# Performance work log

Hardware: AMD Instinct MI355X
Metric: run time of the kernel (lower is better)

The kernel has to match this reference:

```python
import jax, jax.numpy as jnp
import numpy as np

# Arbitrary non-contiguous kernel tap offsets (constructor arg sk_ind)
SK_IND = np.array([-512, -256, -128, -96, -64, -48, -32, -24, -16, -12, -8, -6,
                   -4, -3, -2, -1, 0, 1, 2, 3, 4, 6, 8, 12, 16, 24, 32, 48,
                   64, 96, 128, 256], dtype=np.int32)
IN_CHANNELS = 64
OUT_CHANNELS = 64
BATCH = 16
INPUT_LEN = 4096


def setup_inputs() -> dict:
    key = jax.random.key(0)
    k1, k2 = jax.random.split(key)
    x = jax.random.normal(k1, (BATCH, IN_CHANNELS, INPUT_LEN), dtype=jnp.float32)
    sk_weights = jax.random.normal(k2, (OUT_CHANNELS, IN_CHANNELS, SK_IND.shape[0]), dtype=jnp.float32)
    return {"x": x, "sk_weights": sk_weights}


def reference(x, sk_weights):
    # x: [B, Cin, L]; sk_weights: [Cout, Cin, K]
    B, C, L = x.shape
    low_pad = max(-int(SK_IND.min()), 0)   # zeros consumed by negative taps
    high_pad = max(int(SK_IND.max()), 0)   # zeros consumed by positive taps
    # Original pads zeros AFTER the signal: [x, zeros(high_pad), zeros(low_pad)];
    # negative numpy indices then wrap into the trailing low_pad zeros.
    padded = jnp.concatenate([x, jnp.zeros((B, C, high_pad + low_pad), x.dtype)], axis=-1)
    padded_len = L + high_pad + low_pad
    idx = SK_IND[:, None] + np.arange(L)                 # [K, L], static
    idx = np.where(idx < 0, padded_len + idx, idx)       # emulate numpy negative-index wrap
    gathered = padded[:, :, idx]                          # [B, Cin, K, L]
    # Per-position GEMM: contract over (Cin, K)
    return jnp.einsum('oik,bikl->bol', sk_weights, gathered)  # [B, Cout, L]
```

## Files before the change

kernel.cpp:

```cpp
#include <hip/hip_runtime.h>


#define B_    16
#define CIN   64
#define COUT  64
#define LEN   4096
#define PAD_LO 512
#define PAD_HI 256
#define LPAD  (LEN + PAD_LO + PAD_HI)
#define NTAP  32

typedef float f32x4 __attribute__((ext_vector_type(4)));
typedef short bf16x8_s __attribute__((ext_vector_type(8)));
typedef __bf16 bf16x8_b __attribute__((ext_vector_type(8)));
typedef unsigned short u16x8 __attribute__((ext_vector_type(8)));

template <typename V>
static __device__ inline auto mfma_16x16x32_bf16(V a, V b, f32x4 c, int)
    -> decltype(__builtin_amdgcn_mfma_f32_16x16x32_bf16(a, b, c, 0, 0, 0)) {
  return __builtin_amdgcn_mfma_f32_16x16x32_bf16(a, b, c, 0, 0, 0);
}
template <typename V>
static __device__ inline f32x4 mfma_16x16x32_bf16(V a, V b, f32x4 c, long) {
  return __builtin_amdgcn_mfma_f32_16x16x32_bf16(
      __builtin_bit_cast(bf16x8_b, a), __builtin_bit_cast(bf16x8_b, b), c, 0, 0, 0);
}

static __device__ inline unsigned short f32_to_bf16_rne(float f) {
  unsigned int u = __builtin_bit_cast(unsigned int, f);
  u += 0x7fffu + ((u >> 16) & 1u);
  return (unsigned short)(u >> 16);
}

static __device__ inline void async_copy16(const void* g, void* l) {
  __builtin_amdgcn_global_load_lds((const __attribute__((address_space(1))) unsigned int*)g,
                                   (__attribute__((address_space(3))) unsigned int*)l, 16, 0, 0);
}

__global__ __launch_bounds__(256) void prep_x(const float* __restrict__ x,
                                              unsigned short* __restrict__ xp) {
  __shared__ float tile[64][65];
  const int b = blockIdx.y;
  const int lp0 = blockIdx.x * 64;
  const int tid = threadIdx.x;
  const bool data = (lp0 >= PAD_LO) && (lp0 < PAD_LO + LEN);
  if (data) {
    const int l0 = lp0 - PAD_LO;
#pragma unroll
    for (int it = 0; it < 4; ++it) {
      const int pidx = it * 256 + tid;
      const int il = pidx >> 4;
      const int lq = (pidx & 15) * 4;
      const float4 v = *(const float4*)&x[(size_t)(b * CIN + il) * LEN + l0 + lq];
      tile[lq + 0][il] = v.x;
      tile[lq + 1][il] = v.y;
      tile[lq + 2][il] = v.z;
      tile[lq + 3][il] = v.w;
    }
  }
  __syncthreads();
#pragma unroll
  for (int it = 0; it < 2; ++it) {
    const int pidx = it * 256 + tid;
    const int ll = pidx >> 3;
    const int i8 = (pidx & 7) * 8;
    u16x8 v = {0, 0, 0, 0, 0, 0, 0, 0};
    if (data) {
#pragma unroll
      for (int j = 0; j < 8; ++j) v[j] = f32_to_bf16_rne(tile[ll][i8 + j]);
    }
    *(u16x8*)&xp[(size_t)(b * LPAD + lp0 + ll) * CIN + i8] = v;
  }
}

__global__ __launch_bounds__(256) void prep_w(const float* __restrict__ w,
                                              unsigned short* __restrict__ wf) {
  const int e = blockIdx.x * 256 + threadIdx.x;
  const int j = e & 7;
  const int lane = (e >> 3) & 63;
  const int m = (e >> 9) & 3;
  const int c = (e >> 11) & 1;
  const int t = e >> 12;
  const int q = lane >> 4, r = lane & 15;
  const int o = m * 16 + r;
  const int i = c * 32 + q * 8 + j;
  wf[e] = f32_to_bf16_rne(w[(size_t)(o * CIN + i) * NTAP + t]);
}

__global__ __launch_bounds__(256, 2) void sconv_main(const unsigned short* __restrict__ xp,
                                                     const unsigned short* __restrict__ wf,
                                                     float* __restrict__ out) {
  constexpr int TAP[NTAP] = {-512, -256, -128, -96, -64, -48, -32, -24, -16, -12, -8,
                             -6,   -4,   -3,   -2,  -1,  0,   1,   2,   3,   4,  6,
                             8,    12,   16,   24,  32,  48,  64,  96,  128, 256};
  __shared__ alignas(16) char smem[81920];

  const int id = blockIdx.x;
  const int b = (id & 7) * 2 + ((id >> 3) & 1);
  const int l0 = (id >> 4) * 128;
  const int lb = l0 + PAD_LO;
  const int tid = threadIdx.x;
  const int wv = tid >> 6, lane = tid & 63;
  const int q = lane >> 4, r = lane & 15;
  const int lh = wv & 1, ch = wv >> 1;

  const char* xbase = (const char*)xp + ((size_t)b * LPAD + lb) * (CIN * 2);
  const char* wbase = (const char*)wf;

  auto stageW = [&](int t) {
    const char* src = wbase + t * 8192;
    char* dst = smem + 65536 + (t & 1) * 8192;
#pragma unroll
    for (int it = 0; it < 2; ++it)
      async_copy16(src + (it * 256 + wv * 64 + lane) * 16,
                   dst + (it * 256 + wv * 64) * 16);
  };
  auto stageB = [&](int a0, int ng) {
    for (int g = wv; g < ng; g += 4) {
      const int ra = a0 + g * 8 + (lane >> 3);
      const int cs = (lane & 7) ^ (ra & 7);
      const int sb = (lb + a0 + g * 8) & 511;
      async_copy16(xbase + (ptrdiff_t)ra * 128 + cs * 16, smem + sb * 128);
    }
  };

  f32x4 acc[4][4] = {};

  stageW(0);
  stageB(-512, 16);

#pragma unroll
  for (int t = 0; t < NTAP; ++t) {
    __syncthreads();
    if (t + 1 < NTAP) {
      stageW(t + 1);
      const int dstart = TAP[t] + 128;
      const int dend = TAP[t + 1] + 128;
      const int a0 = dstart & ~7;
      stageB(a0, (dend - a0 + 7) >> 3);
    }
    __builtin_amdgcn_sched_barrier(0);

    const int e = (TAP[t] + r) & 7;
    const char* Wb = smem + 65536 + (t & 1) * 8192 + ch * 4096;
    bf16x8_s A[4], Bf[4];
#pragma unroll
    for (int m = 0; m < 4; ++m)
      A[m] = *(const bf16x8_s*)(Wb + m * 1024 + lane * 16);
#pragma unroll
    for (int n = 0; n < 4; ++n) {
      const int slot = (lb + TAP[t] + lh * 64 + 16 * n + r) & 511;
      Bf[n] = *(const bf16x8_s*)(smem + slot * 128 + (((ch * 4 + q) ^ e) << 4));
    }
#pragma unroll
    for (int m = 0; m < 4; ++m)
#pragma unroll
      for (int n = 0; n < 4; ++n)
        acc[m][n] = mfma_16x16x32_bf16(A[m], Bf[n], acc[m][n], 0);
  }

  __syncthreads();
  if (ch == 1) {
#pragma unroll
    for (int m = 0; m < 4; ++m)
#pragma unroll
      for (int n = 0; n < 4; ++n)
        *(f32x4*)(smem + lh * 16384 + ((m * 4 + n) * 64 + lane) * 16) = acc[m][n];
  }
  __syncthreads();
  if (ch == 0) {
#pragma unroll
    for (int m = 0; m < 4; ++m)
#pragma unroll
      for (int n = 0; n < 4; ++n) {
        const f32x4 other = *(const f32x4*)(smem + lh * 16384 + ((m * 4 + n) * 64 + lane) * 16);
        const f32x4 v = acc[m][n] + other;
#pragma unroll
        for (int d = 0; d < 4; ++d) {
          const int o = 16 * m + 4 * q + d;
          const int l = l0 + lh * 64 + 16 * n + r;
          out[((size_t)b * COUT + o) * LEN + l] = v[d];
        }
      }
  }
}

extern "C" void kernel_launch(void* const* d_in, const int* in_sizes, int n_in,
                              void* d_out, int out_size, void* d_ws, size_t ws_size,
                              hipStream_t stream) {
  const float* x = (const float*)d_in[0];
  const float* w = (const float*)d_in[1];
  float* out = (float*)d_out;

  unsigned short* xp = (unsigned short*)d_ws;
  unsigned short* wfp = xp + (size_t)B_ * LPAD * CIN;

  prep_x<<<dim3(LPAD / 64, B_), 256, 0, stream>>>(x, xp);
  prep_w<<<dim3((NTAP * 2 * 4 * 64 * 8) / 256), 256, 0, stream>>>(w, wfp);
  sconv_main<<<dim3(16 * 32), 256, 0, stream>>>(xp, wfp, out);
}
```

Before: 92.50 us.

## Use larger 256-position tiles with register double-buffered fragments and deeper prefetch

Each block now covers 256 output positions with 8 waves instead of 128 positions with 4 waves, using a 1024-row LDS ring for the shifted input rows. The weight and halo prefetch runs two taps ahead, and the LDS fragment reads for the next tap are loaded into a second register set while the current tap's MFMAs issue. The goal is to hide LDS read latency behind the matrix ops and to reduce redundant halo loads per output. The cost is about 144KB of LDS per block, which allows only one block per CU, plus higher register pressure from the doubled fragment sets.

```diff
diff --git a/kernel.cpp b/kernel.cpp
--- a/kernel.cpp
+++ b/kernel.cpp
@@ -9,6 +9,7 @@
 #define PAD_HI 256
 #define LPAD  (LEN + PAD_LO + PAD_HI)
 #define NTAP  32
+#define WOFF  131072
 
 typedef float f32x4 __attribute__((ext_vector_type(4)));
 typedef short bf16x8_s __attribute__((ext_vector_type(8)));
@@ -87,76 +88,80 @@
   wf[e] = f32_to_bf16_rne(w[(size_t)(o * CIN + i) * NTAP + t]);
 }
 
-__global__ __launch_bounds__(256, 2) void sconv_main(const unsigned short* __restrict__ xp,
+__global__ __launch_bounds__(512, 2) void sconv_main(const unsigned short* __restrict__ xp,
                                                      const unsigned short* __restrict__ wf,
                                                      float* __restrict__ out) {
   constexpr int TAP[NTAP] = {-512, -256, -128, -96, -64, -48, -32, -24, -16, -12, -8,
                              -6,   -4,   -3,   -2,  -1,  0,   1,   2,   3,   4,  6,
                              8,    12,   16,   24,  32,  48,  64,  96,  128, 256};
-  __shared__ alignas(16) char smem[81920];
+  __shared__ alignas(16) char smem[WOFF + 16384];
 
   const int id = blockIdx.x;
-  const int b = (id & 7) * 2 + ((id >> 3) & 1);
-  const int l0 = (id >> 4) * 128;
+  const int b = (id & 7) * 2 + (id >> 7);
+  const int l0 = ((id >> 3) & 15) * 256;
   const int lb = l0 + PAD_LO;
   const int tid = threadIdx.x;
   const int wv = tid >> 6, lane = tid & 63;
   const int q = lane >> 4, r = lane & 15;
-  const int lh = wv & 1, ch = wv >> 1;
+  const int lh = wv >> 1, ch = wv & 1;
 
   const char* xbase = (const char*)xp + ((size_t)b * LPAD + lb) * (CIN * 2);
   const char* wbase = (const char*)wf;
 
   auto stageW = [&](int t) {
-    const char* src = wbase + t * 8192;
-    char* dst = smem + 65536 + (t & 1) * 8192;
-#pragma unroll
-    for (int it = 0; it < 2; ++it)
-      async_copy16(src + (it * 256 + wv * 64 + lane) * 16,
-                   dst + (it * 256 + wv * 64) * 16);
+    async_copy16(wbase + t * 8192 + (wv * 64 + lane) * 16,
+                 smem + WOFF + (t & 1) * 8192 + wv * 1024);
   };
   auto stageB = [&](int a0, int ng) {
-    for (int g = wv; g < ng; g += 4) {
+    for (int g = wv; g < ng; g += 8) {
       const int ra = a0 + g * 8 + (lane >> 3);
       const int cs = (lane & 7) ^ (ra & 7);
-      const int sb = (lb + a0 + g * 8) & 511;
+      const int sb = (lb + a0 + g * 8) & 1023;
       async_copy16(xbase + (ptrdiff_t)ra * 128 + cs * 16, smem + sb * 128);
     }
   };
 
   f32x4 acc[4][4] = {};
+  bf16x8_s Ab[2][4], Bb[2][4];
+
+  auto readFrags = [&](int tt, int p) {
+    const char* Wb = smem + WOFF + (tt & 1) * 8192 + ch * 4096;
+#pragma unroll
+    for (int m = 0; m < 4; ++m)
+      Ab[p][m] = *(const bf16x8_s*)(Wb + m * 1024 + lane * 16);
+    const int e = (TAP[tt] + r) & 7;
+#pragma unroll
+    for (int n = 0; n < 4; ++n) {
+      const int slot = (lb + TAP[tt] + lh * 64 + 16 * n + r) & 1023;
+      Bb[p][n] = *(const bf16x8_s*)(smem + slot * 128 + (((ch * 4 + q) ^ e) << 4));
+    }
+  };
 
   stageW(0);
-  stageB(-512, 16);
+  stageW(1);
+  stageB(-512, 64);
+  __syncthreads();
+  readFrags(0, 0);
 
 #pragma unroll
   for (int t = 0; t < NTAP; ++t) {
     __syncthreads();
-    if (t + 1 < NTAP) {
-      stageW(t + 1);
-      const int dstart = TAP[t] + 128;
-      const int dend = TAP[t + 1] + 128;
+    if (t + 2 < NTAP) {
+      stageW(t + 2);
+      const int dstart = TAP[t + 1] + 256;
+      const int dend = TAP[t + 2] + 256;
       const int a0 = dstart & ~7;
       stageB(a0, (dend - a0 + 7) >> 3);
     }
     __builtin_amdgcn_sched_barrier(0);
-
-    const int e = (TAP[t] + r) & 7;
-    const char* Wb = smem + 65536 + (t & 1) * 8192 + ch * 4096;
-    bf16x8_s A[4], Bf[4];
-#pragma unroll
-    for (int m = 0; m < 4; ++m)
-      A[m] = *(const bf16x8_s*)(Wb + m * 1024 + lane * 16);
-#pragma unroll
-    for (int n = 0; n < 4; ++n) {
-      const int slot = (lb + TAP[t] + lh * 64 + 16 * n + r) & 511;
-      Bf[n] = *(const bf16x8_s*)(smem + slot * 128 + (((ch * 4 + q) ^ e) << 4));
-    }
+    if (t + 1 < NTAP) readFrags(t + 1, (t + 1) & 1);
+    __builtin_amdgcn_sched_barrier(0);
+    const int p = t & 1;
 #pragma unroll
     for (int m = 0; m < 4; ++m)
 #pragma unroll
       for (int n = 0; n < 4; ++n)
-        acc[m][n] = mfma_16x16x32_bf16(A[m], Bf[n], acc[m][n], 0);
+        acc[m][n] = mfma_16x16x32_bf16(Ab[p][m], Bb[p][n], acc[m][n], 0);
   }
 
   __syncthreads();
@@ -197,5 +202,5 @@
 
   prep_x<<<dim3(LPAD / 64, B_), 256, 0, stream>>>(x, xp);
   prep_w<<<dim3((NTAP * 2 * 4 * 64 * 8) / 256), 256, 0, stream>>>(w, wfp);
-  sconv_main<<<dim3(16 * 32), 256, 0, stream>>>(xp, wfp, out);
-}
+  sconv_main<<<dim3(256), 512, 0, stream>>>(xp, wfp, out);
+}
```

Result: no change. 93.53 us (+1.1%).
